# Performance work log

Measured on AMD Instinct MI355X. Metric: run time of the kernel, lower is better.

Reference implementation:

```python
import jax, jax.numpy as jnp
import numpy as np

B, C, H, W, NH = 2, 192, 256, 256, 4


def setup_inputs() -> dict:
    key = jax.random.key(0)
    k0, k1, k2, k3 = jax.random.split(key, 4)
    x = jax.random.normal(k0, (B, C, H, W), jnp.float32)
    qkv_w = jax.random.normal(k1, (3 * C, C), jnp.float32) * 0.02      # 1x1 conv as matmul
    dw_w = jax.random.normal(k2, (3 * C, 1, 3, 3), jnp.float32) * 0.02  # depthwise 3x3, groups=3C
    proj_w = jax.random.normal(k3, (C, C), jnp.float32) * 0.02          # 1x1 output conv
    temperature = jnp.ones((NH, 1, 1), jnp.float32)
    return dict(x=x, qkv_w=qkv_w, dw_w=dw_w, proj_w=proj_w, temperature=temperature)


def reference(x, qkv_w, dw_w, proj_w, temperature):
    b, c, hgt, wid = x.shape
    nh = temperature.shape[0]
    hd = c // nh  # head channel dim

    # 1x1 pointwise qkv projection (Conv2d(C, 3C, 1, bias=False))
    qkv = jnp.einsum('bchw,oc->bohw', x, qkv_w)
    # 3x3 depthwise conv, groups = 3C, padding=1
    qkv = jax.lax.conv_general_dilated(
        qkv, dw_w, window_strides=(1, 1), padding='SAME',
        dimension_numbers=('NCHW', 'OIHW', 'NCHW'),
        feature_group_count=3 * c)

    q, k, v = jnp.split(qkv, 3, axis=1)
    # b (h c) x y -> b h c (x y)
    q = q.reshape(b, nh, hd, hgt * wid)
    k = k.reshape(b, nh, hd, hgt * wid)
    v = v.reshape(b, nh, hd, hgt * wid)

    # F.normalize(dim=-1): L2 normalize over spatial axis, eps clamp like torch
    eps = 1e-12
    q = q / jnp.maximum(jnp.linalg.norm(q, axis=-1, keepdims=True), eps)
    k = k / jnp.maximum(jnp.linalg.norm(k, axis=-1, keepdims=True), eps)

    # CxC channel attention per head, scaled by learned temperature
    attn = jnp.einsum('bhcn,bhdn->bhcd', q, k) * temperature  # [b, nh, hd, hd]
    attn = jax.nn.softmax(attn, axis=-1)
    out = jnp.einsum('bhcd,bhdn->bhcn', attn, v)

    # b h c (x y) -> b (h c) x y
    out = out.reshape(b, c, hgt, wid)
    # 1x1 output projection
    return jnp.einsum('bchw,oc->bohw', out, proj_w)
```

## Files before the change

kernel.cpp:

```cpp
#include <hip/hip_runtime.h>

typedef __attribute__((ext_vector_type(8))) short short8;
typedef __attribute__((ext_vector_type(4))) float f32x4;
typedef __attribute__((ext_vector_type(4))) unsigned short u16x4;

#define B_   2
#define C_   192
#define NH_  4
#define HD_  48
#define CO_  576
#define HGT_ 256
#define WID_ 256
#define NSP_ 65536

__device__ __forceinline__ unsigned short f2bf(float f) {
  unsigned int u = __float_as_uint(f);
  u += 0x7FFFu + ((u >> 16) & 1u);
  return (unsigned short)(u >> 16);
}
__device__ __forceinline__ float bf2f(unsigned short h) {
  return __uint_as_float(((unsigned int)h) << 16);
}
__device__ __forceinline__ int swz(int n) { return (n & 7) ^ ((n >> 3) & 7); }

__global__ void k_cvtA(const float* __restrict__ src, unsigned short* __restrict__ dst) {
  int i = blockIdx.x * 256 + threadIdx.x;
  if (i >= CO_ * C_) return;
  int m = i / C_, k = i % C_;
  int f = m >> 4, l15 = m & 15, kk = k >> 5, lg = (k >> 3) & 3, j = k & 7;
  dst[((((f * 6 + kk) * 4 + lg) * 16 + l15) << 3) + j] = f2bf(src[i]);
}

__global__ __launch_bounds__(256)
void k_cvtX(const float* __restrict__ src, unsigned short* __restrict__ dst, int n8) {
  int i = blockIdx.x * 256 + threadIdx.x;
  if (i >= n8) return;
  const float4* s = (const float4*)src + (size_t)i * 2;
  float4 a = s[0], b = s[1];
  short8 o;
  o[0] = (short)f2bf(a.x); o[1] = (short)f2bf(a.y); o[2] = (short)f2bf(a.z); o[3] = (short)f2bf(a.w);
  o[4] = (short)f2bf(b.x); o[5] = (short)f2bf(b.y); o[6] = (short)f2bf(b.z); o[7] = (short)f2bf(b.w);
  *(short8*)(dst + (size_t)i * 8) = o;
}

template<int MBLOCKS, int TPB, bool OUT_BF16>
__global__ __launch_bounds__(256, 2)
void k_gemm(const unsigned short* __restrict__ Aperm, long aBatchStride,
            const unsigned short* __restrict__ Xin, long xBatchStride, int xChanOff,
            void* __restrict__ Out, long outBatchStride)
{
  constexpr int NSETX = 1024 / TPB / 8;
  __shared__ unsigned short Xs[192 * 72];
  const int tid = threadIdx.x;
  const int b = blockIdx.z;
  int mb, nset;
  {
    int orig = blockIdx.x;
    int xcd = orig & 7, wid = orig >> 3;
    if (MBLOCKS == 3) { mb = wid % 3; nset = xcd * NSETX + wid / 3; }
    else              { mb = 0;       nset = xcd * NSETX + wid; }
  }

  const int sn = tid & 15, sk = tid >> 4;
  const int n0 = sn * 4, hh = sk & 1;
  const unsigned short* Xb = Xin + (size_t)b * xBatchStride + (size_t)xChanOff * NSP_;

  const int wave = tid >> 6, lane = tid & 63;
  const int l15 = lane & 15, lg = lane >> 4;
  const int fragM0 = mb * 12 + wave * 3;
  const unsigned short* Ap = Aperm + (size_t)b * aBatchStride;

  short8 af[6][3];
#pragma unroll
  for (int kk = 0; kk < 6; kk++)
#pragma unroll
    for (int fm = 0; fm < 3; fm++)
      af[kk][fm] = *(const short8*)(Ap + (((size_t)((fragM0 + fm) * 6 + kk) * 64 + lane) << 3));

  u16x4 rh[3][4];
  auto LOADT = [&](int nb) {
    const size_t cb = (size_t)nb * 64 + n0;
#pragma unroll
    for (int it = 0; it < 3; it++) {
      const unsigned short* p = Xb + (size_t)(it * 64 + sk * 4) * NSP_ + cb;
#pragma unroll
      for (int r = 0; r < 4; r++) rh[it][r] = *(const u16x4*)(p + (size_t)r * NSP_);
    }
  };
  auto WRITEC = [&]() {
#pragma unroll
    for (int it = 0; it < 3; it++) {
      const int u16v = it * 8 + (sk >> 1);
#pragma unroll
      for (int j = 0; j < 4; j++) {
        int n = n0 + j;
        u16x4 w;
        w[0] = rh[it][0][j]; w[1] = rh[it][1][j]; w[2] = rh[it][2][j]; w[3] = rh[it][3][j];
        *(u16x4*)&Xs[n * 192 + ((u16v ^ swz(n)) << 3) + (hh << 2)] = w;
      }
    }
  };

  LOADT(nset * TPB);
  for (int t = 0; t < TPB; t++) {
    const int nb = nset * TPB + t;
    WRITEC();
    asm volatile("s_waitcnt lgkmcnt(0)" ::: "memory");
    __builtin_amdgcn_s_barrier();
    if (t + 1 < TPB) LOADT(nb + 1);

    f32x4 acc[3][4];
#pragma unroll
    for (int i = 0; i < 3; i++)
#pragma unroll
      for (int j = 0; j < 4; j++) acc[i][j] = (f32x4){0.f, 0.f, 0.f, 0.f};

#pragma unroll
    for (int kk = 0; kk < 6; kk++) {
      const int ur = kk * 4 + lg;
      short8 bfr[4];
#pragma unroll
      for (int fn = 0; fn < 4; fn++) {
        int col = fn * 16 + l15;
        bfr[fn] = *(const short8*)(&Xs[col * 192 + ((ur ^ swz(col)) << 3)]);
      }
      __builtin_amdgcn_s_setprio(1);
#pragma unroll
      for (int fm = 0; fm < 3; fm++)
#pragma unroll
        for (int fn = 0; fn < 4; fn++)
          acc[fm][fn] = __builtin_amdgcn_mfma_f32_16x16x32_bf16(bfr[fn], af[kk][fm], acc[fm][fn], 0, 0, 0);
      __builtin_amdgcn_s_setprio(0);
    }

    if (OUT_BF16) {
      asm volatile("s_waitcnt lgkmcnt(0)" ::: "memory");
      __builtin_amdgcn_s_barrier();
#pragma unroll
      for (int fm = 0; fm < 3; fm++) {
        int mloc = (wave * 3 + fm) * 16 + l15;
#pragma unroll
        for (int fn = 0; fn < 4; fn++) {
          u16x4 w;
          w[0] = f2bf(acc[fm][fn][0]); w[1] = f2bf(acc[fm][fn][1]);
          w[2] = f2bf(acc[fm][fn][2]); w[3] = f2bf(acc[fm][fn][3]);
          *(u16x4*)&Xs[mloc * 72 + fn * 16 + lg * 4] = w;
        }
      }
      asm volatile("s_waitcnt lgkmcnt(0)" ::: "memory");
      __builtin_amdgcn_s_barrier();
      unsigned short* O = (unsigned short*)Out + (size_t)b * outBatchStride +
                          (size_t)mb * 192 * NSP_ + (size_t)nb * 64;
#pragma unroll
      for (int i = 0; i < 6; i++) {
        int p = tid + i * 256, row = p >> 3, cB = (p & 7) * 8;
        short8 v = *(const short8*)&Xs[row * 72 + cB];
        *(short8*)(O + (size_t)row * NSP_ + cB) = v;
      }
      asm volatile("s_waitcnt lgkmcnt(0)" ::: "memory");
      __builtin_amdgcn_s_barrier();
    } else {
      float* O = (float*)Out + (size_t)b * outBatchStride;
      const size_t ncol0 = (size_t)nb * 64;
#pragma unroll
      for (int fm = 0; fm < 3; fm++) {
        int m = (fragM0 + fm) * 16 + l15;
#pragma unroll
        for (int fn = 0; fn < 4; fn++)
          *(f32x4*)(O + (size_t)m * NSP_ + ncol0 + fn * 16 + lg * 4) = acc[fm][fn];
      }
      asm volatile("s_waitcnt lgkmcnt(0)" ::: "memory");
      __builtin_amdgcn_s_barrier();
    }
  }
}

#define DW_RT 16
__global__ __launch_bounds__(256)
void k_dw(const unsigned short* __restrict__ qkv, const float* __restrict__ dww,
          unsigned short* __restrict__ out, float* __restrict__ sumsq)
{
  const int ch = blockIdx.y;
  const int b  = blockIdx.z;
  const int tid = threadIdx.x;
  const int seg = tid & 31;
  const int rb  = tid >> 5;
  const int ybase = blockIdx.x * (8 * DW_RT) + rb * DW_RT;

  const unsigned short* in = qkv + ((size_t)b * CO_ + ch) * NSP_;
  unsigned short* o = out + ((size_t)b * CO_ + ch) * NSP_;
  float w[9];
#pragma unroll
  for (int i = 0; i < 9; i++) w[i] = dww[ch * 9 + i];

  float rw[3][10];
  float ss = 0.f;
#pragma unroll
  for (int i = 0; i < DW_RT + 2; i++) {
    const int yy = ybase - 1 + i;
    float* f = rw[i % 3];
    if ((unsigned)yy < (unsigned)HGT_) {
      short8 v = *(const short8*)(in + (size_t)yy * WID_ + seg * 8);
#pragma unroll
      for (int j = 0; j < 8; j++) f[j + 1] = bf2f((unsigned short)v[j]);
    } else {
#pragma unroll
      for (int j = 0; j < 8; j++) f[j + 1] = 0.f;
    }
    float lf = __shfl_up(f[8], 1, 32);
    float rt = __shfl_down(f[1], 1, 32);
    f[0] = (seg == 0)  ? 0.f : lf;
    f[9] = (seg == 31) ? 0.f : rt;
    if (i >= 2) {
      const float* a  = rw[(i - 2) % 3];
      const float* bb = rw[(i - 1) % 3];
      const float* cc = f;
      short8 ov;
#pragma unroll
      for (int j = 0; j < 8; j++) {
        float acc = a[j]  * w[0] + a[j + 1]  * w[1] + a[j + 2]  * w[2]
                  + bb[j] * w[3] + bb[j + 1] * w[4] + bb[j + 2] * w[5]
                  + cc[j] * w[6] + cc[j + 1] * w[7] + cc[j + 2] * w[8];
        ov[j] = (short)f2bf(acc);
        ss += acc * acc;
      }
      *(short8*)(o + (size_t)(yy - 1) * WID_ + seg * 8) = ov;
    }
  }

  if (ch < 2 * C_) {
#pragma unroll
    for (int off = 32; off > 0; off >>= 1) ss += __shfl_down(ss, off);
    __shared__ float wsum[4];
    if ((tid & 63) == 0) wsum[tid >> 6] = ss;
    __syncthreads();
    if (tid == 0) atomicAdd(&sumsq[b * 2 * C_ + ch], wsum[0] + wsum[1] + wsum[2] + wsum[3]);
  }
}

__global__ __launch_bounds__(256)
void k_qk(const unsigned short* __restrict__ qkvd, float* __restrict__ part)
{
  const int chunk = blockIdx.x;
  const int h = blockIdx.y, b = blockIdx.z;
  const int tid = threadIdx.x;
  const int wave = tid >> 6, lane = tid & 63;
  const int l15 = lane & 15, lg = lane >> 4;
  const unsigned short* qb = qkvd + (size_t)b * CO_ * NSP_ + (size_t)(h * HD_) * NSP_;
  const unsigned short* kb = qkvd + (size_t)b * CO_ * NSP_ + (size_t)(C_ + h * HD_) * NSP_;
  const int kbase = chunk * 1024 + wave * 256;

  f32x4 acc[3][3];
#pragma unroll
  for (int i = 0; i < 3; i++)
#pragma unroll
    for (int j = 0; j < 3; j++) acc[i][j] = (f32x4){0.f, 0.f, 0.f, 0.f};

#pragma unroll
  for (int ks = 0; ks < 8; ks++) {
    const int k0 = kbase + ks * 32 + lg * 8;
    short8 af[3], bfr[3];
#pragma unroll
    for (int i = 0; i < 3; i++)
      af[i] = *(const short8*)(qb + (size_t)(i * 16 + l15) * NSP_ + k0);
#pragma unroll
    for (int i = 0; i < 3; i++)
      bfr[i] = *(const short8*)(kb + (size_t)(i * 16 + l15) * NSP_ + k0);
#pragma unroll
    for (int fm = 0; fm < 3; fm++)
#pragma unroll
      for (int fn = 0; fn < 3; fn++)
        acc[fm][fn] = __builtin_amdgcn_mfma_f32_16x16x32_bf16(af[fm], bfr[fn], acc[fm][fn], 0, 0, 0);
  }

  __shared__ float red[4][HD_ * HD_];
#pragma unroll
  for (int fm = 0; fm < 3; fm++)
#pragma unroll
    for (int fn = 0; fn < 3; fn++)
#pragma unroll
      for (int r = 0; r < 4; r++)
        red[wave][(fm * 16 + lg * 4 + r) * HD_ + fn * 16 + l15] = acc[fm][fn][r];
  __syncthreads();

  float* P = part + ((size_t)(b * NH_ + h) * 64 + chunk) * (HD_ * HD_);
#pragma unroll
  for (int j = 0; j < 9; j++) {
    int e = tid + j * 256;
    P[e] = red[0][e] + red[1][e] + red[2][e] + red[3][e];
  }
}

__global__ __launch_bounds__(256)
void k_smax(const float* __restrict__ part, const float* __restrict__ sumsq,
            const float* __restrict__ temp, const float* __restrict__ projw,
            unsigned short* __restrict__ M)
{
  const int h = blockIdx.x, b = blockIdx.y;
  const int tid = threadIdx.x;
  __shared__ float lgt[HD_][HD_];
  __shared__ float at[HD_][HD_];
  __shared__ float pw[C_][HD_];
  const float tmp = temp[h];
  const float* P = part + (size_t)(b * NH_ + h) * 64 * (HD_ * HD_);

  float s[9];
#pragma unroll
  for (int j = 0; j < 9; j++) s[j] = 0.f;
  for (int p = 0; p < 64; p++) {
    const float* Pp = P + (size_t)p * (HD_ * HD_);
#pragma unroll
    for (int j = 0; j < 9; j++) s[j] += Pp[tid + j * 256];
  }
#pragma unroll
  for (int j = 0; j < 9; j++) {
    int e = tid + j * 256;
    int c = e / HD_, d = e % HD_;
    float nq = fmaxf(sqrtf(sumsq[b * 2 * C_ + h * HD_ + c]), 1e-12f);
    float nk = fmaxf(sqrtf(sumsq[b * 2 * C_ + C_ + h * HD_ + d]), 1e-12f);
    lgt[c][d] = s[j] / (nq * nk) * tmp;
  }
  for (int e = tid; e < C_ * HD_; e += 256) {
    int o = e / HD_, c = e % HD_;
    pw[o][c] = projw[o * C_ + h * HD_ + c];
  }
  __syncthreads();
  if (tid < HD_) {
    float mx = -1e30f;
    for (int d = 0; d < HD_; d++) mx = fmaxf(mx, lgt[tid][d]);
    float ssum = 0.f;
    for (int d = 0; d < HD_; d++) { float e_ = expf(lgt[tid][d] - mx); at[tid][d] = e_; ssum += e_; }
    float inv = 1.f / ssum;
    for (int d = 0; d < HD_; d++) at[tid][d] *= inv;
  }
  __syncthreads();
  unsigned short* Mo = M + (size_t)b * C_ * C_;
  for (int e = tid; e < C_ * HD_; e += 256) {
    int o = e / HD_, d = e % HD_;
    float sm = 0.f;
    for (int c = 0; c < HD_; c++) sm += pw[o][c] * at[c][d];
    int col = h * HD_ + d;
    int f = o >> 4, l15 = o & 15, kk = col >> 5, lg = (col >> 3) & 3, j = col & 7;
    Mo[((((f * 6 + kk) * 4 + lg) * 16 + l15) << 3) + j] = f2bf(sm);
  }
}

extern "C" void kernel_launch(void* const* d_in, const int* in_sizes, int n_in,
                              void* d_out, int out_size, void* d_ws, size_t ws_size,
                              hipStream_t stream)
{
  const float* x     = (const float*)d_in[0];
  const float* qkvw  = (const float*)d_in[1];
  const float* dww   = (const float*)d_in[2];
  const float* projw = (const float*)d_in[3];
  const float* temp  = (const float*)d_in[4];
  float* out         = (float*)d_out;

  char* ws = (char*)d_ws;
  size_t off = 0;
  auto alloc = [&](size_t bytes) { void* p = ws + off; off += (bytes + 255) & ~(size_t)255; return p; };
  unsigned short* qkvd_bf = (unsigned short*)alloc((size_t)B_ * CO_ * NSP_ * 2);
  unsigned short* qkv_bf  = (unsigned short*)alloc((size_t)B_ * CO_ * NSP_ * 2);
  unsigned short* qkvw_bf = (unsigned short*)alloc((size_t)CO_ * C_ * 2);
  unsigned short* M_bf    = (unsigned short*)alloc((size_t)B_ * C_ * C_ * 2);
  float* sumsq            = (float*)alloc((size_t)B_ * 2 * C_ * 4);
  float* part             = (float*)alloc((size_t)B_ * NH_ * 64 * HD_ * HD_ * 4);
  unsigned short* x_bf    = qkvd_bf;

  hipMemsetAsync(sumsq, 0, (size_t)B_ * 2 * C_ * 4, stream);
  k_cvtA<<<dim3((CO_ * C_ + 255) / 256), dim3(256), 0, stream>>>(qkvw, qkvw_bf);
  k_cvtX<<<dim3(B_ * C_ * NSP_ / 8 / 256), dim3(256), 0, stream>>>(x, x_bf, B_ * C_ * NSP_ / 8);
  k_gemm<3, 8, true><<<dim3(384, 1, B_), dim3(256), 0, stream>>>(
      qkvw_bf, 0, x_bf, (long)C_ * NSP_, 0, qkv_bf, (long)CO_ * NSP_);
  k_dw<<<dim3(HGT_ / (8 * DW_RT), CO_, B_), dim3(256), 0, stream>>>(qkv_bf, dww, qkvd_bf, sumsq);
  k_qk<<<dim3(64, NH_, B_), dim3(256), 0, stream>>>(qkvd_bf, part);
  k_smax<<<dim3(NH_, B_), dim3(256), 0, stream>>>(part, sumsq, temp, projw, M_bf);
  k_gemm<1, 4, false><<<dim3(256, 1, B_), dim3(256), 0, stream>>>(
      M_bf, (long)C_ * C_, qkvd_bf, (long)CO_ * NSP_, 2 * C_, out, (long)C_ * NSP_);
}
```

Before: 251.6 us.

## Fuse fp32-to-bf16 input conversion into QKV GEMM and stage depthwise rows in LDS

Drops the separate x conversion kernel. The first GEMM now loads fp32 x directly and rounds it to bf16 while writing the LDS tile, which removes one full write and re-read of a bf16 copy of x. The depthwise conv kernel is restructured so each block loads 34 halo rows into shared memory once, instead of each 16-row strip reloading its own halo rows and using shuffles for the left and right neighbours. The GEMM loads twice as many bytes per tile and does the conversion inside its loop, and the depthwise blocks are now smaller and use LDS.

```diff
diff --git a/kernel.cpp b/kernel.cpp
--- a/kernel.cpp
+++ b/kernel.cpp
@@ -31,22 +31,10 @@
   dst[((((f * 6 + kk) * 4 + lg) * 16 + l15) << 3) + j] = f2bf(src[i]);
 }
 
-__global__ __launch_bounds__(256)
-void k_cvtX(const float* __restrict__ src, unsigned short* __restrict__ dst, int n8) {
-  int i = blockIdx.x * 256 + threadIdx.x;
-  if (i >= n8) return;
-  const float4* s = (const float4*)src + (size_t)i * 2;
-  float4 a = s[0], b = s[1];
-  short8 o;
-  o[0] = (short)f2bf(a.x); o[1] = (short)f2bf(a.y); o[2] = (short)f2bf(a.z); o[3] = (short)f2bf(a.w);
-  o[4] = (short)f2bf(b.x); o[5] = (short)f2bf(b.y); o[6] = (short)f2bf(b.z); o[7] = (short)f2bf(b.w);
-  *(short8*)(dst + (size_t)i * 8) = o;
-}
-
-template<int MBLOCKS, int TPB, bool OUT_BF16>
+template<int MBLOCKS, int TPB, bool X_BF16, bool OUT_BF16>
 __global__ __launch_bounds__(256, 2)
 void k_gemm(const unsigned short* __restrict__ Aperm, long aBatchStride,
-            const unsigned short* __restrict__ Xin, long xBatchStride, int xChanOff,
+            const void* __restrict__ Xin, long xBatchStride, int xChanOff,
             void* __restrict__ Out, long outBatchStride)
 {
   constexpr int NSETX = 1024 / TPB / 8;
@@ -63,7 +51,8 @@
 
   const int sn = tid & 15, sk = tid >> 4;
   const int n0 = sn * 4, hh = sk & 1;
-  const unsigned short* Xb = Xin + (size_t)b * xBatchStride + (size_t)xChanOff * NSP_;
+  const float* Xf = (const float*)Xin + (size_t)b * xBatchStride + (size_t)xChanOff * NSP_;
+  const unsigned short* Xh = (const unsigned short*)Xin + (size_t)b * xBatchStride + (size_t)xChanOff * NSP_;
 
   const int wave = tid >> 6, lane = tid & 63;
   const int l15 = lane & 15, lg = lane >> 4;
@@ -77,14 +66,21 @@
     for (int fm = 0; fm < 3; fm++)
       af[kk][fm] = *(const short8*)(Ap + (((size_t)((fragM0 + fm) * 6 + kk) * 64 + lane) << 3));
 
+  f32x4 rf[3][4];
   u16x4 rh[3][4];
   auto LOADT = [&](int nb) {
     const size_t cb = (size_t)nb * 64 + n0;
 #pragma unroll
     for (int it = 0; it < 3; it++) {
-      const unsigned short* p = Xb + (size_t)(it * 64 + sk * 4) * NSP_ + cb;
-#pragma unroll
-      for (int r = 0; r < 4; r++) rh[it][r] = *(const u16x4*)(p + (size_t)r * NSP_);
+      if (!X_BF16) {
+        const float* p = Xf + (size_t)(it * 64 + sk * 4) * NSP_ + cb;
+#pragma unroll
+        for (int r = 0; r < 4; r++) rf[it][r] = *(const f32x4*)(p + (size_t)r * NSP_);
+      } else {
+        const unsigned short* p = Xh + (size_t)(it * 64 + sk * 4) * NSP_ + cb;
+#pragma unroll
+        for (int r = 0; r < 4; r++) rh[it][r] = *(const u16x4*)(p + (size_t)r * NSP_);
+      }
     }
   };
   auto WRITEC = [&]() {
@@ -95,7 +91,10 @@
       for (int j = 0; j < 4; j++) {
         int n = n0 + j;
         u16x4 w;
-        w[0] = rh[it][0][j]; w[1] = rh[it][1][j]; w[2] = rh[it][2][j]; w[3] = rh[it][3][j];
+        if (!X_BF16) { w[0] = f2bf(rf[it][0][j]); w[1] = f2bf(rf[it][1][j]);
+                       w[2] = f2bf(rf[it][2][j]); w[3] = f2bf(rf[it][3][j]); }
+        else         { w[0] = rh[it][0][j]; w[1] = rh[it][1][j];
+                       w[2] = rh[it][2][j]; w[3] = rh[it][3][j]; }
         *(u16x4*)&Xs[n * 192 + ((u16v ^ swz(n)) << 3) + (hh << 2)] = w;
       }
     }
@@ -175,17 +174,16 @@
   }
 }
 
-#define DW_RT 16
-__global__ __launch_bounds__(256)
+#define DW_RB 32
+__global__ __launch_bounds__(256, 6)
 void k_dw(const unsigned short* __restrict__ qkv, const float* __restrict__ dww,
           unsigned short* __restrict__ out, float* __restrict__ sumsq)
 {
+  __shared__ unsigned short rows[34][272];
   const int ch = blockIdx.y;
   const int b  = blockIdx.z;
   const int tid = threadIdx.x;
-  const int seg = tid & 31;
-  const int rb  = tid >> 5;
-  const int ybase = blockIdx.x * (8 * DW_RT) + rb * DW_RT;
+  const int ybase = blockIdx.x * DW_RB;
 
   const unsigned short* in = qkv + ((size_t)b * CO_ + ch) * NSP_;
   unsigned short* o = out + ((size_t)b * CO_ + ch) * NSP_;
@@ -193,27 +191,45 @@
 #pragma unroll
   for (int i = 0; i < 9; i++) w[i] = dww[ch * 9 + i];
 
-  float rw[3][10];
+  short8 st[5];
+#pragma unroll
+  for (int i = 0; i < 5; i++) {
+    int u = tid + i * 256;
+    if (u < 1088) {
+      int r = u >> 5, sg = u & 31;
+      int yy = ybase - 1 + r;
+      short8 z = {0, 0, 0, 0, 0, 0, 0, 0};
+      if ((unsigned)yy < (unsigned)HGT_) z = *(const short8*)(in + (size_t)yy * WID_ + sg * 8);
+      st[i] = z;
+    }
+  }
+#pragma unroll
+  for (int i = 0; i < 5; i++) {
+    int u = tid + i * 256;
+    if (u < 1088) {
+      int r = u >> 5, sg = u & 31;
+      *(short8*)&rows[r][8 + sg * 8] = st[i];
+    }
+  }
+  if (tid < 68) rows[tid >> 1][(tid & 1) ? 264 : 7] = 0;
+  __syncthreads();
+
+  const int seg = tid & 31, rowblk = tid >> 5;
+  const int c0 = 8 + seg * 8;
+  float win[3][10];
   float ss = 0.f;
 #pragma unroll
-  for (int i = 0; i < DW_RT + 2; i++) {
-    const int yy = ybase - 1 + i;
-    float* f = rw[i % 3];
-    if ((unsigned)yy < (unsigned)HGT_) {
-      short8 v = *(const short8*)(in + (size_t)yy * WID_ + seg * 8);
-#pragma unroll
-      for (int j = 0; j < 8; j++) f[j + 1] = bf2f((unsigned short)v[j]);
-    } else {
-#pragma unroll
-      for (int j = 0; j < 8; j++) f[j + 1] = 0.f;
-    }
-    float lf = __shfl_up(f[8], 1, 32);
-    float rt = __shfl_down(f[1], 1, 32);
-    f[0] = (seg == 0)  ? 0.f : lf;
-    f[9] = (seg == 31) ? 0.f : rt;
+  for (int i = 0; i < 6; i++) {
+    const int lr = rowblk * 4 + i;
+    float* f = win[i % 3];
+    short8 v = *(const short8*)&rows[lr][c0];
+#pragma unroll
+    for (int j = 0; j < 8; j++) f[j + 1] = bf2f((unsigned short)v[j]);
+    f[0] = bf2f(rows[lr][c0 - 1]);
+    f[9] = bf2f(rows[lr][c0 + 8]);
     if (i >= 2) {
-      const float* a  = rw[(i - 2) % 3];
-      const float* bb = rw[(i - 1) % 3];
+      const float* a  = win[(i - 2) % 3];
+      const float* bb = win[(i - 1) % 3];
       const float* cc = f;
       short8 ov;
 #pragma unroll
@@ -224,7 +240,7 @@
         ov[j] = (short)f2bf(acc);
         ss += acc * acc;
       }
-      *(short8*)(o + (size_t)(yy - 1) * WID_ + seg * 8) = ov;
+      *(short8*)(o + (size_t)(ybase + rowblk * 4 + i - 2) * WID_ + seg * 8) = ov;
     }
   }
 
@@ -365,16 +381,14 @@
   unsigned short* M_bf    = (unsigned short*)alloc((size_t)B_ * C_ * C_ * 2);
   float* sumsq            = (float*)alloc((size_t)B_ * 2 * C_ * 4);
   float* part             = (float*)alloc((size_t)B_ * NH_ * 64 * HD_ * HD_ * 4);
-  unsigned short* x_bf    = qkvd_bf;
 
   hipMemsetAsync(sumsq, 0, (size_t)B_ * 2 * C_ * 4, stream);
   k_cvtA<<<dim3((CO_ * C_ + 255) / 256), dim3(256), 0, stream>>>(qkvw, qkvw_bf);
-  k_cvtX<<<dim3(B_ * C_ * NSP_ / 8 / 256), dim3(256), 0, stream>>>(x, x_bf, B_ * C_ * NSP_ / 8);
-  k_gemm<3, 8, true><<<dim3(384, 1, B_), dim3(256), 0, stream>>>(
-      qkvw_bf, 0, x_bf, (long)C_ * NSP_, 0, qkv_bf, (long)CO_ * NSP_);
-  k_dw<<<dim3(HGT_ / (8 * DW_RT), CO_, B_), dim3(256), 0, stream>>>(qkv_bf, dww, qkvd_bf, sumsq);
+  k_gemm<3, 8, false, true><<<dim3(384, 1, B_), dim3(256), 0, stream>>>(
+      qkvw_bf, 0, x, (long)C_ * NSP_, 0, qkv_bf, (long)CO_ * NSP_);
+  k_dw<<<dim3(HGT_ / DW_RB, CO_, B_), dim3(256), 0, stream>>>(qkv_bf, dww, qkvd_bf, sumsq);
   k_qk<<<dim3(64, NH_, B_), dim3(256), 0, stream>>>(qkvd_bf, part);
   k_smax<<<dim3(NH_, B_), dim3(256), 0, stream>>>(part, sumsq, temp, projw, M_bf);
-  k_gemm<1, 4, false><<<dim3(256, 1, B_), dim3(256), 0, stream>>>(
+  k_gemm<1, 4, true, false><<<dim3(256, 1, B_), dim3(256), 0, stream>>>(
       M_bf, (long)C_ * C_, qkvd_bf, (long)CO_ * NSP_, 2 * C_, out, (long)C_ * NSP_);
 }
```

Result: faster. 224.2 us (median of 2 runs) (-10.9%).
